# Performance work log

Hardware: AMD Instinct MI355X
Metric: run time of the kernel (lower is better)

The kernel has to match this reference:

```python
import jax, jax.numpy as jnp
import numpy as np

EPS = 1e-5

def _bn(x, g, b):
    # training-mode BatchNorm1d: batch statistics (biased variance), eps=1e-5
    mean = jnp.mean(x, axis=0)
    var = jnp.mean(jnp.square(x - mean), axis=0)
    return (x - mean) * jax.lax.rsqrt(var + EPS) * g + b

def setup_inputs() -> dict:
    key = jax.random.key(0)
    ks = jax.random.split(key, 16)
    n_nodes, n_edges, d_h, d_e = 50000, 800000, 128, 64
    in_feats, h1, h2, out_feats = 2 * d_h + d_e, 256, 128, 1
    def lin(k, fi, fo):
        bound = 1.0 / np.sqrt(fi)
        kw, kb = jax.random.split(k)
        W = jax.random.uniform(kw, (fo, fi), jnp.float32, -bound, bound)
        b = jax.random.uniform(kb, (fo,), jnp.float32, -bound, bound)
        return W, b
    W1, b1 = lin(ks[0], in_feats, h1)
    W2, b2 = lin(ks[1], h1, h2)
    W3, b3 = lin(ks[2], h2, out_feats)
    return {
        "h": jax.random.normal(ks[3], (n_nodes, d_h), jnp.float32),
        "e": jax.random.normal(ks[4], (n_edges, d_e), jnp.float32),
        "src": jax.random.randint(ks[5], (n_edges,), 0, n_nodes, jnp.int32),
        "dst": jax.random.randint(ks[6], (n_edges,), 0, n_nodes, jnp.int32),
        "bn0_g": jnp.ones((in_feats,), jnp.float32), "bn0_b": jnp.zeros((in_feats,), jnp.float32),
        "W1": W1, "b1": b1,
        "bn1_g": jnp.ones((h1,), jnp.float32), "bn1_b": jnp.zeros((h1,), jnp.float32),
        "W2": W2, "b2": b2,
        "bn2_g": jnp.ones((h2,), jnp.float32), "bn2_b": jnp.zeros((h2,), jnp.float32),
        "W3": W3, "b3": b3,
    }

def reference(h, e, src, dst, bn0_g, bn0_b, W1, b1, bn1_g, bn1_b, W2, b2, bn2_g, bn2_b, W3, b3):
    # edge gather + concat: [n_edges, 2*d_h + d_e]
    x = jnp.concatenate([h[src], h[dst], e], axis=1)
    x = _bn(x, bn0_g, bn0_b)
    x = jnp.maximum(x @ W1.T + b1, 0.0)  # Linear + ReLU (dropout = identity, deterministic)
    x = _bn(x, bn1_g, bn1_b)
    x = jnp.maximum(x @ W2.T + b2, 0.0)
    x = _bn(x, bn2_g, bn2_b)
    return x @ W3.T + b3
```

## Files before the change

kernel.cpp:

```cpp
#include <hip/hip_runtime.h>


#define N_EDGES 800000
#define N_NODES 50000

typedef __attribute__((ext_vector_type(8))) short bf8_t;
typedef __attribute__((ext_vector_type(4))) float f4_t;
typedef __attribute__((ext_vector_type(2))) unsigned int u2_t;
typedef __attribute__((ext_vector_type(4))) unsigned int u4_t;

__device__ __forceinline__ unsigned short f2bf(float f) {
    unsigned int u = __builtin_bit_cast(unsigned int, f);
    u += 0x7FFFu + ((u >> 16) & 1u);
    return (unsigned short)(u >> 16);
}
__device__ __forceinline__ float bf2f(unsigned short s) {
    unsigned int u = ((unsigned int)s) << 16;
    return __builtin_bit_cast(float, u);
}
__device__ __forceinline__ unsigned int cvt_pk(float lo, float hi) {
    unsigned int r;
    asm("v_cvt_pk_bf16_f32 %0, %1, %2" : "=v"(r) : "v"(lo), "v"(hi));
    return r;
}
__device__ __forceinline__ bf8_t cvt8(f4_t x, f4_t y) {
    union { unsigned int u[4]; bf8_t v; } r;
    r.u[0] = cvt_pk(x[0], x[1]);
    r.u[1] = cvt_pk(x[2], x[3]);
    r.u[2] = cvt_pk(y[0], y[1]);
    r.u[3] = cvt_pk(y[2], y[3]);
    return r.v;
}

__global__ __launch_bounds__(256) void k_hist(const int* __restrict__ src, const int* __restrict__ dst,
                                              int* __restrict__ cs, int* __restrict__ cd) {
    int i = blockIdx.x * 256 + threadIdx.x;
    if (i < N_EDGES) {
        atomicAdd(&cs[src[i]], 1);
        atomicAdd(&cd[dst[i]], 1);
    }
}

__global__ __launch_bounds__(256) void k_ecvt(const float* __restrict__ e,
        unsigned short* __restrict__ ebf, float* __restrict__ sum, float* __restrict__ sq) {
    const int tid = threadIdx.x;
    const int lane = tid & 63;
    const int cg = tid & 7, rr = tid >> 3;
    f4_t sa = {0.f,0.f,0.f,0.f}, sb = sa, qa = sa, qb = sa;
    for (int r = blockIdx.x * 32 + rr; r < N_EDGES; r += gridDim.x * 32) {
        f4_t va = __builtin_nontemporal_load((const f4_t*)(e + (size_t)r * 64 + cg * 8));
        f4_t vb = __builtin_nontemporal_load((const f4_t*)(e + (size_t)r * 64 + cg * 8 + 4));
        sa += va; qa += va * va; sb += vb; qb += vb * vb;
        bf8_t o = cvt8(va, vb);
        __builtin_nontemporal_store(o,
            (bf8_t*)(ebf + (size_t)(r >> 4) * 1024 + (cg >> 2) * 512 + (((r & 15) << 2) + (cg & 3)) * 8));
    }
#pragma unroll
    for (int d = 8; d <= 32; d <<= 1) {
#pragma unroll
        for (int j = 0; j < 4; ++j) {
            sa[j] += __shfl_xor(sa[j], d); qa[j] += __shfl_xor(qa[j], d);
            sb[j] += __shfl_xor(sb[j], d); qb[j] += __shfl_xor(qb[j], d);
        }
    }
    __shared__ float red[128];
    if (tid < 128) red[tid] = 0.f;
    __syncthreads();
    if (lane < 8) {
#pragma unroll
        for (int j = 0; j < 4; ++j) {
            atomicAdd(&red[lane * 8 + j], sa[j]);
            atomicAdd(&red[lane * 8 + 4 + j], sb[j]);
            atomicAdd(&red[64 + lane * 8 + j], qa[j]);
            atomicAdd(&red[64 + lane * 8 + 4 + j], qb[j]);
        }
    }
    __syncthreads();
    if (tid < 64) atomicAdd(&sum[256 + tid], red[tid]);
    else if (tid < 128) atomicAdd(&sq[256 + tid - 64], red[tid]);
}

__global__ __launch_bounds__(256) void k_hstats(const float* __restrict__ h,
                                                const int* __restrict__ cs, const int* __restrict__ cd,
                                                float* __restrict__ sum, float* __restrict__ sq) {
    const int tid = threadIdx.x;
    const int c = tid & 127, g = tid >> 7;
    float ss = 0.f, qs = 0.f, sd = 0.f, qd = 0.f;
    for (int n = blockIdx.x * 2 + g; n < N_NODES; n += gridDim.x * 2) {
        float v = h[(size_t)n * 128 + c];
        float a = (float)cs[n], b = (float)cd[n];
        ss += a * v; qs += a * v * v;
        sd += b * v; qd += b * v * v;
    }
    __shared__ float red[256];
    red[tid] = ss; __syncthreads();
    if (tid < 128) atomicAdd(&sum[tid], red[tid] + red[tid + 128]);
    __syncthreads();
    red[tid] = qs; __syncthreads();
    if (tid < 128) atomicAdd(&sq[tid], red[tid] + red[tid + 128]);
    __syncthreads();
    red[tid] = sd; __syncthreads();
    if (tid < 128) atomicAdd(&sum[128 + tid], red[tid] + red[tid + 128]);
    __syncthreads();
    red[tid] = qd; __syncthreads();
    if (tid < 128) atomicAdd(&sq[128 + tid], red[tid] + red[tid + 128]);
}

__global__ __launch_bounds__(320) void k_fold0(const float* __restrict__ sum, const float* __restrict__ sq,
        const float* __restrict__ g0, const float* __restrict__ b0,
        float* __restrict__ scale0, float* __restrict__ shift0) {
    int j = threadIdx.x;
    if (j < 320) {
        const float invE = 1.f / (float)N_EDGES;
        float mu = sum[j] * invE;
        float var = sq[j] * invE - mu * mu;
        float sc = g0[j] * rsqrtf(var + 1e-5f);
        scale0[j] = sc;
        shift0[j] = b0[j] - mu * sc;
    }
}

__global__ __launch_bounds__(320) void k_foldW1(const float* __restrict__ W1, const float* __restrict__ b1,
        const float* __restrict__ scale0, const float* __restrict__ shift0,
        unsigned short* __restrict__ W1s, unsigned short* __restrict__ W1d,
        unsigned short* __restrict__ W1e, float* __restrict__ b1p) {
    __shared__ float sc[320], sh[320];
    const int tid = threadIdx.x;
    if (tid < 320) { sc[tid] = scale0[tid]; sh[tid] = shift0[tid]; }
    __syncthreads();
    if (tid < 256) {
        float acc = b1[tid];
        const float* wr = W1 + (size_t)tid * 320;
        for (int j = 0; j < 320; ++j) {
            float wv = wr[j];
            acc += wv * sh[j];
            unsigned short wb = f2bf(wv * sc[j]);
            if (j < 128) W1s[tid * 128 + j] = wb;
            else if (j < 256) W1d[tid * 128 + (j - 128)] = wb;
            else W1e[tid * 64 + (j - 256)] = wb;
        }
        b1p[tid] = acc;
    }
}

__global__ __launch_bounds__(256) void k_P(const float* __restrict__ h,
        const unsigned short* __restrict__ W1s, const unsigned short* __restrict__ W1d,
        unsigned short* __restrict__ Ps, unsigned short* __restrict__ Pd) {
    __shared__ unsigned short tile[16 * 264];
    const int tid = threadIdx.x;
    const int w = tid >> 6, lane = tid & 63, quad = lane >> 4, l15 = lane & 15;
    const unsigned short* W = blockIdx.y ? W1d : W1s;
    unsigned short* P = blockIdx.y ? Pd : Ps;
    const size_t base = (size_t)blockIdx.x * 256;
    bf8_t bfr[4][4];
#pragma unroll
    for (int j = 0; j < 4; ++j) {
        const unsigned short* wp = W + (size_t)((w * 4 + j) * 16 + l15) * 128 + quad * 8;
#pragma unroll
        for (int ks = 0; ks < 4; ++ks) bfr[j][ks] = *(const bf8_t*)(wp + ks * 32);
    }
    const int erow = tid >> 4, ex = tid & 15;
    for (int mc = 0; mc < 16; ++mc) {
        const size_t row0 = base + mc * 16;
        size_t ar = row0 + l15; if (ar >= N_NODES) ar = N_NODES - 1;
        const float* hp = h + ar * 128 + quad * 8;
        bf8_t af[4];
#pragma unroll
        for (int ks = 0; ks < 4; ++ks)
            af[ks] = cvt8(*(const f4_t*)(hp + ks * 32), *(const f4_t*)(hp + ks * 32 + 4));
#pragma unroll
        for (int j = 0; j < 4; ++j) {
            f4_t t = {0.f, 0.f, 0.f, 0.f};
#pragma unroll
            for (int ks = 0; ks < 4; ++ks)
                t = __builtin_amdgcn_mfma_f32_16x16x32_bf16(af[ks], bfr[j][ks], t, 0, 0, 0);
            const unsigned int p01 = cvt_pk(t[0], t[1]);
            const unsigned int p23 = cvt_pk(t[2], t[3]);
            const int col = (w * 4 + j) * 16 + l15;
            tile[(quad * 4 + 0) * 264 + col] = (unsigned short)p01;
            tile[(quad * 4 + 1) * 264 + col] = (unsigned short)(p01 >> 16);
            tile[(quad * 4 + 2) * 264 + col] = (unsigned short)p23;
            tile[(quad * 4 + 3) * 264 + col] = (unsigned short)(p23 >> 16);
        }
        __syncthreads();
        const size_t orow = row0 + erow;
        if (orow < N_NODES) {
            u4_t v0 = *(const u4_t*)(tile + erow * 264 + ex * 16);
            u4_t v1 = *(const u4_t*)(tile + erow * 264 + ex * 16 + 8);
            *(u4_t*)(P + orow * 256 + ex * 16) = v0;
            *(u4_t*)(P + orow * 256 + ex * 16 + 8) = v1;
        }
        __syncthreads();
    }
}

__global__ __launch_bounds__(256) void k_stats1(const unsigned short* __restrict__ ebf,
        const int* __restrict__ src, const int* __restrict__ dst,
        const unsigned short* __restrict__ Ps, const unsigned short* __restrict__ Pd,
        const unsigned short* __restrict__ W1e, const float* __restrict__ b1p,
        float* __restrict__ slots) {
    __shared__ __align__(16) float tile1[2][16 * 268];
    __shared__ int sIdx[256], dIdx[256];
    const int tid = threadIdx.x;
    const int w = tid >> 6, lane = tid & 63, quad = lane >> 4, l15 = lane & 15;
    const int perm = l15 * 4 + quad;
    const size_t base = (size_t)blockIdx.x * 256;
    const size_t blk16 = (size_t)blockIdx.x * 16;
    sIdx[tid] = src[base + tid];
    dIdx[tid] = dst[base + tid];
    bf8_t bfr1[4][2];
    float bias4[4];
#pragma unroll
    for (int j = 0; j < 4; ++j) {
        const unsigned short* wp = W1e + (size_t)((w * 4 + j) * 16 + l15) * 64 + quad * 8;
        bfr1[j][0] = *(const bf8_t*)(wp);
        bfr1[j][1] = *(const bf8_t*)(wp + 32);
        bias4[j] = b1p[(w * 4 + j) * 16 + l15];
    }
    const int erow = tid >> 4, ex = tid & 15;
    float s[16], q[16];
#pragma unroll
    for (int j = 0; j < 16; ++j) { s[j] = 0.f; q[j] = 0.f; }
    __syncthreads();
    bf8_t af0, af1;
    u4_t gs0, gs1, gd0, gd1;
    {
        const unsigned short* ap = ebf + blk16 * 1024 + perm * 8;
        af0 = __builtin_nontemporal_load((const bf8_t*)(ap));
        af1 = __builtin_nontemporal_load((const bf8_t*)(ap + 512));
        const size_t sr = (size_t)sIdx[erow] * 256, dr = (size_t)dIdx[erow] * 256;
        gs0 = *(const u4_t*)(Ps + sr + ex * 8);
        gs1 = *(const u4_t*)(Ps + sr + ex * 8 + 128);
        gd0 = *(const u4_t*)(Pd + dr + ex * 8);
        gd1 = *(const u4_t*)(Pd + dr + ex * 8 + 128);
    }
    for (int mc = 0; mc < 16; ++mc) {
        float* t1 = tile1[mc & 1];
#pragma unroll
        for (int j = 0; j < 4; ++j) {
            f4_t t = {bias4[j], bias4[j], bias4[j], bias4[j]};
            t = __builtin_amdgcn_mfma_f32_16x16x32_bf16(af0, bfr1[j][0], t, 0, 0, 0);
            t = __builtin_amdgcn_mfma_f32_16x16x32_bf16(af1, bfr1[j][1], t, 0, 0, 0);
#pragma unroll
            for (int r = 0; r < 4; ++r)
                t1[(quad * 4 + r) * 268 + (w * 4 + j) * 16 + l15] = t[r];
        }
        if (mc < 15) {
            const unsigned short* ap = ebf + (blk16 + mc + 1) * 1024 + perm * 8;
            af0 = __builtin_nontemporal_load((const bf8_t*)(ap));
            af1 = __builtin_nontemporal_load((const bf8_t*)(ap + 512));
        }
        __syncthreads();
#pragma unroll
        for (int i = 0; i < 2; ++i) {
            const float* tp = t1 + erow * 268 + ex * 8 + 128 * i;
            f4_t tv0 = *(const f4_t*)tp;
            f4_t tv1 = *(const f4_t*)(tp + 4);
            const unsigned short* su = (const unsigned short*)(i ? &gs1 : &gs0);
            const unsigned short* du = (const unsigned short*)(i ? &gd1 : &gd0);
#pragma unroll
            for (int j = 0; j < 4; ++j) {
                float v = fmaxf(tv0[j] + bf2f(su[j]) + bf2f(du[j]), 0.f);
                s[i * 8 + j] += v; q[i * 8 + j] += v * v;
            }
#pragma unroll
            for (int j = 0; j < 4; ++j) {
                float v = fmaxf(tv1[j] + bf2f(su[4 + j]) + bf2f(du[4 + j]), 0.f);
                s[i * 8 + 4 + j] += v; q[i * 8 + 4 + j] += v * v;
            }
        }
        if (mc < 15) {
            const size_t sr = (size_t)sIdx[(mc + 1) * 16 + erow] * 256;
            const size_t dr = (size_t)dIdx[(mc + 1) * 16 + erow] * 256;
            gs0 = *(const u4_t*)(Ps + sr + ex * 8);
            gs1 = *(const u4_t*)(Ps + sr + ex * 8 + 128);
            gd0 = *(const u4_t*)(Pd + dr + ex * 8);
            gd1 = *(const u4_t*)(Pd + dr + ex * 8 + 128);
        }
    }
#pragma unroll
    for (int j = 0; j < 16; ++j) {
        s[j] += __shfl_xor(s[j], 16); s[j] += __shfl_xor(s[j], 32);
        q[j] += __shfl_xor(q[j], 16); q[j] += __shfl_xor(q[j], 32);
    }
    float* scratch = &tile1[0][0];
    if (lane < 16) {
#pragma unroll
        for (int j = 0; j < 16; ++j) {
            scratch[(w * 16 + l15) * 16 + j] = s[j];
            scratch[1024 + (w * 16 + l15) * 16 + j] = q[j];
        }
    }
    __syncthreads();
    {
        const int c = tid;
        const int idx = (c & 7) + (c >> 7) * 8;
        const int exx = (c >> 3) & 15;
        float S = 0.f, Q = 0.f;
#pragma unroll
        for (int ww = 0; ww < 4; ++ww) {
            S += scratch[(ww * 16 + exx) * 16 + idx];
            Q += scratch[1024 + (ww * 16 + exx) * 16 + idx];
        }
        float* sl = slots + (size_t)(blockIdx.x & 63) * 512;
        atomicAdd(&sl[c], S);
        atomicAdd(&sl[256 + c], Q);
    }
}

__global__ __launch_bounds__(256) void k_fold1(const float* __restrict__ slots,
        const float* __restrict__ g1, const float* __restrict__ b1n,
        const float* __restrict__ W2, const float* __restrict__ b2,
        unsigned short* __restrict__ W2p, float* __restrict__ b2p) {
    __shared__ float sc[256], sh[256];
    const int tid = threadIdx.x;
    float S = 0.f, Q = 0.f;
    for (int s = 0; s < 64; ++s) { S += slots[s * 512 + tid]; Q += slots[s * 512 + 256 + tid]; }
    const float invE = 1.f / (float)N_EDGES;
    float mu = S * invE;
    float var = Q * invE - mu * mu;
    float scl = g1[tid] * rsqrtf(var + 1e-5f);
    sc[tid] = scl; sh[tid] = b1n[tid] - mu * scl;
    __syncthreads();
    if (tid < 128) {
        float acc = b2[tid];
        const float* wr = W2 + (size_t)tid * 256;
        for (int j = 0; j < 256; ++j) {
            float wv = wr[j];
            acc += wv * sh[j];
            W2p[tid * 256 + j] = f2bf(wv * sc[j]);
        }
        b2p[tid] = acc;
    }
}

__global__ __launch_bounds__(256) void k_L12(const unsigned short* __restrict__ ebf,
        const int* __restrict__ src, const int* __restrict__ dst,
        const unsigned short* __restrict__ Ps, const unsigned short* __restrict__ Pd,
        const unsigned short* __restrict__ W1e, const float* __restrict__ b1p,
        const unsigned short* __restrict__ W2p, const float* __restrict__ b2p,
        unsigned short* __restrict__ a2c, float* __restrict__ slots) {
    __shared__ __align__(16) float tile1[16 * 268];
    __shared__ unsigned short tile2[2][4096];
    __shared__ int sIdx[256], dIdx[256];
    const int tid = threadIdx.x;
    const int w = tid >> 6, lane = tid & 63, quad = lane >> 4, l15 = lane & 15;
    const int perm = l15 * 4 + quad;
    const size_t base = (size_t)blockIdx.x * 256;
    const size_t blk16 = (size_t)blockIdx.x * 16;
    sIdx[tid] = src[base + tid];
    dIdx[tid] = dst[base + tid];
    bf8_t bfr1[4][2];
    float bias4[4];
#pragma unroll
    for (int j = 0; j < 4; ++j) {
        const unsigned short* wp = W1e + (size_t)((w * 4 + j) * 16 + l15) * 64 + quad * 8;
        bfr1[j][0] = *(const bf8_t*)(wp);
        bfr1[j][1] = *(const bf8_t*)(wp + 32);
        bias4[j] = b1p[(w * 4 + j) * 16 + l15];
    }
    bf8_t bfr2[2][8];
    float bias2[2];
#pragma unroll
    for (int j = 0; j < 2; ++j) {
        const unsigned short* wp = W2p + (size_t)((w * 2 + j) * 16 + l15) * 256 + quad * 8;
#pragma unroll
        for (int ks = 0; ks < 8; ++ks) bfr2[j][ks] = *(const bf8_t*)(wp + ks * 32);
        bias2[j] = b2p[(w * 2 + j) * 16 + l15];
    }
    const int erow = tid >> 4, ex = tid & 15;
    float s0 = 0.f, q0 = 0.f, s1 = 0.f, q1 = 0.f;
    __syncthreads();
    bf8_t af0, af1;
    u4_t gs0, gs1, gd0, gd1;
    {
        const unsigned short* ap = ebf + blk16 * 1024 + perm * 8;
        af0 = __builtin_nontemporal_load((const bf8_t*)(ap));
        af1 = __builtin_nontemporal_load((const bf8_t*)(ap + 512));
        const size_t sr = (size_t)sIdx[erow] * 256, dr = (size_t)dIdx[erow] * 256;
        gs0 = *(const u4_t*)(Ps + sr + ex * 8);
        gs1 = *(const u4_t*)(Ps + sr + ex * 8 + 128);
        gd0 = *(const u4_t*)(Pd + dr + ex * 8);
        gd1 = *(const u4_t*)(Pd + dr + ex * 8 + 128);
    }
    for (int mc = 0; mc < 16; ++mc) {
        unsigned short* t2 = tile2[mc & 1];
#pragma unroll
        for (int j = 0; j < 4; ++j) {
            f4_t t = {bias4[j], bias4[j], bias4[j], bias4[j]};
            t = __builtin_amdgcn_mfma_f32_16x16x32_bf16(af0, bfr1[j][0], t, 0, 0, 0);
            t = __builtin_amdgcn_mfma_f32_16x16x32_bf16(af1, bfr1[j][1], t, 0, 0, 0);
#pragma unroll
            for (int r = 0; r < 4; ++r)
                tile1[(quad * 4 + r) * 268 + (w * 4 + j) * 16 + l15] = t[r];
        }
        if (mc < 15) {
            const unsigned short* ap = ebf + (blk16 + mc + 1) * 1024 + perm * 8;
            af0 = __builtin_nontemporal_load((const bf8_t*)(ap));
            af1 = __builtin_nontemporal_load((const bf8_t*)(ap + 512));
        }
        __syncthreads();
#pragma unroll
        for (int i = 0; i < 2; ++i) {
            const float* tp = tile1 + erow * 268 + ex * 8 + 128 * i;
            f4_t tv0 = *(const f4_t*)tp;
            f4_t tv1 = *(const f4_t*)(tp + 4);
            const unsigned short* su = (const unsigned short*)(i ? &gs1 : &gs0);
            const unsigned short* du = (const unsigned short*)(i ? &gd1 : &gd0);
            float c0 = fmaxf(tv0[0] + bf2f(su[0]) + bf2f(du[0]), 0.f);
            float c1 = fmaxf(tv0[1] + bf2f(su[1]) + bf2f(du[1]), 0.f);
            float c2 = fmaxf(tv0[2] + bf2f(su[2]) + bf2f(du[2]), 0.f);
            float c3 = fmaxf(tv0[3] + bf2f(su[3]) + bf2f(du[3]), 0.f);
            float c4 = fmaxf(tv1[0] + bf2f(su[4]) + bf2f(du[4]), 0.f);
            float c5 = fmaxf(tv1[1] + bf2f(su[5]) + bf2f(du[5]), 0.f);
            float c6 = fmaxf(tv1[2] + bf2f(su[6]) + bf2f(du[6]), 0.f);
            float c7 = fmaxf(tv1[3] + bf2f(su[7]) + bf2f(du[7]), 0.f);
            u4_t ov;
            ov[0] = cvt_pk(c0, c1);
            ov[1] = cvt_pk(c2, c3);
            ov[2] = cvt_pk(c4, c5);
            ov[3] = cvt_pk(c6, c7);
            *(u4_t*)(&t2[((ex >> 2) + 4 * i) * 512 + (erow * 4 + (ex & 3)) * 8]) = ov;
        }
        if (mc < 15) {
            const size_t sr = (size_t)sIdx[(mc + 1) * 16 + erow] * 256;
            const size_t dr = (size_t)dIdx[(mc + 1) * 16 + erow] * 256;
            gs0 = *(const u4_t*)(Ps + sr + ex * 8);
            gs1 = *(const u4_t*)(Ps + sr + ex * 8 + 128);
            gd0 = *(const u4_t*)(Pd + dr + ex * 8);
            gd1 = *(const u4_t*)(Pd + dr + ex * 8 + 128);
        }
        __syncthreads();
        f4_t acc0 = {bias2[0], bias2[0], bias2[0], bias2[0]};
        f4_t acc1 = {bias2[1], bias2[1], bias2[1], bias2[1]};
#pragma unroll
        for (int ks = 0; ks < 8; ++ks) {
            bf8_t a = *(const bf8_t*)(&t2[ks * 512 + perm * 8]);
            acc0 = __builtin_amdgcn_mfma_f32_16x16x32_bf16(a, bfr2[0][ks], acc0, 0, 0, 0);
            acc1 = __builtin_amdgcn_mfma_f32_16x16x32_bf16(a, bfr2[1][ks], acc1, 0, 0, 0);
        }
        unsigned short* outp = a2c + (blk16 + mc) * 2048;
        {
            float v0 = fmaxf(acc0[0], 0.f), v1 = fmaxf(acc0[1], 0.f);
            float v2 = fmaxf(acc0[2], 0.f), v3 = fmaxf(acc0[3], 0.f);
            s0 += v0; q0 += v0 * v0; s0 += v1; q0 += v1 * v1;
            s0 += v2; q0 += v2 * v2; s0 += v3; q0 += v3 * v3;
            u2_t pw; pw[0] = cvt_pk(v0, v1); pw[1] = cvt_pk(v2, v3);
            __builtin_nontemporal_store(pw,
                (u2_t*)(outp + (((w * 2) * 16 + l15) * 4 + quad) * 4));
        }
        {
            float v0 = fmaxf(acc1[0], 0.f), v1 = fmaxf(acc1[1], 0.f);
            float v2 = fmaxf(acc1[2], 0.f), v3 = fmaxf(acc1[3], 0.f);
            s1 += v0; q1 += v0 * v0; s1 += v1; q1 += v1 * v1;
            s1 += v2; q1 += v2 * v2; s1 += v3; q1 += v3 * v3;
            u2_t pw; pw[0] = cvt_pk(v0, v1); pw[1] = cvt_pk(v2, v3);
            __builtin_nontemporal_store(pw,
                (u2_t*)(outp + (((w * 2 + 1) * 16 + l15) * 4 + quad) * 4));
        }
    }
    s0 += __shfl_xor(s0, 16); s0 += __shfl_xor(s0, 32);
    q0 += __shfl_xor(q0, 16); q0 += __shfl_xor(q0, 32);
    s1 += __shfl_xor(s1, 16); s1 += __shfl_xor(s1, 32);
    q1 += __shfl_xor(q1, 16); q1 += __shfl_xor(q1, 32);
    if (lane < 16) {
        float* sl = slots + (size_t)(blockIdx.x & 63) * 256;
        const int c0 = (w * 2) * 16 + l15;
        atomicAdd(&sl[c0], s0); atomicAdd(&sl[128 + c0], q0);
        atomicAdd(&sl[c0 + 16], s1); atomicAdd(&sl[128 + c0 + 16], q1);
    }
}

__global__ __launch_bounds__(128) void k_fold2(const float* __restrict__ slots,
        const float* __restrict__ g2, const float* __restrict__ b2n,
        const float* __restrict__ W3, const float* __restrict__ b3,
        float* __restrict__ w3p, float* __restrict__ b3p) {
    __shared__ float red[128];
    const int tid = threadIdx.x;
    float S = 0.f, Q = 0.f;
    for (int s = 0; s < 64; ++s) { S += slots[s * 256 + tid]; Q += slots[s * 256 + 128 + tid]; }
    const float invE = 1.f / (float)N_EDGES;
    float mu = S * invE;
    float var = Q * invE - mu * mu;
    float scl = g2[tid] * rsqrtf(var + 1e-5f);
    float shf = b2n[tid] - mu * scl;
    w3p[tid] = W3[tid] * scl;
    red[tid] = W3[tid] * shf;
    __syncthreads();
    for (int st = 64; st > 0; st >>= 1) {
        if (tid < st) red[tid] += red[tid + st];
        __syncthreads();
    }
    if (tid == 0) b3p[0] = b3[0] + red[0];
}

__global__ __launch_bounds__(256) void k_L3(const unsigned short* __restrict__ a2c,
        const float* __restrict__ w3p, const float* __restrict__ b3p, float* __restrict__ out) {
    __shared__ float wl[128];
    const int tid = threadIdx.x;
    if (tid < 128) wl[tid] = w3p[tid];
    __syncthreads();
    const int w = tid >> 6, lane = tid & 63, q = lane >> 4, c = lane & 15;
    const float bb = b3p[0];
#pragma unroll
    for (int i = 0; i < 4; ++i) {
        const size_t b = (size_t)blockIdx.x * 16 + w * 4 + i;
        const unsigned short* bp = a2c + b * 2048 + c * 16 + q * 4;
        float a0 = 0.f, a1r = 0.f, a2r = 0.f, a3r = 0.f;
#pragma unroll
        for (int jt = 0; jt < 8; ++jt) {
            u2_t v = __builtin_nontemporal_load((const u2_t*)(bp + jt * 256));
            const unsigned short* u = (const unsigned short*)&v;
            const float wv = wl[jt * 16 + c];
            a0 += bf2f(u[0]) * wv; a1r += bf2f(u[1]) * wv;
            a2r += bf2f(u[2]) * wv; a3r += bf2f(u[3]) * wv;
        }
#pragma unroll
        for (int d = 1; d <= 8; d <<= 1) {
            a0 += __shfl_xor(a0, d); a1r += __shfl_xor(a1r, d);
            a2r += __shfl_xor(a2r, d); a3r += __shfl_xor(a3r, d);
        }
        if (c == 0) {
            f4_t o = {a0 + bb, a1r + bb, a2r + bb, a3r + bb};
            *(f4_t*)(out + b * 16 + q * 4) = o;
        }
    }
}

extern "C" void kernel_launch(void* const* d_in, const int* in_sizes, int n_in,
                              void* d_out, int out_size, void* d_ws, size_t ws_size,
                              hipStream_t stream) {
    (void)in_sizes; (void)n_in; (void)out_size; (void)ws_size;
    const float* h   = (const float*)d_in[0];
    const float* e   = (const float*)d_in[1];
    const int*   src = (const int*)d_in[2];
    const int*   dst = (const int*)d_in[3];
    const float* bn0_g = (const float*)d_in[4];
    const float* bn0_b = (const float*)d_in[5];
    const float* W1 = (const float*)d_in[6];
    const float* b1 = (const float*)d_in[7];
    const float* bn1_g = (const float*)d_in[8];
    const float* bn1_b = (const float*)d_in[9];
    const float* W2 = (const float*)d_in[10];
    const float* b2 = (const float*)d_in[11];
    const float* bn2_g = (const float*)d_in[12];
    const float* bn2_b = (const float*)d_in[13];
    const float* W3 = (const float*)d_in[14];
    const float* b3 = (const float*)d_in[15];

    char* ws = (char*)d_ws;
    size_t off = 0;
    auto alloc = [&](size_t bytes) { char* p = ws + off; off += (bytes + 255) & ~(size_t)255; return p; };
    int*   cnt_s = (int*)alloc((size_t)N_NODES * 4);
    int*   cnt_d = (int*)alloc((size_t)N_NODES * 4);
    float* bn0_sum = (float*)alloc(320 * 4);
    float* bn0_sq  = (float*)alloc(320 * 4);
    float* bn1_slots = (float*)alloc(64 * 512 * 4);
    float* bn2_slots = (float*)alloc(64 * 256 * 4);
    const size_t zero_end = off;
    float* scale0 = (float*)alloc(320 * 4);
    float* shift0 = (float*)alloc(320 * 4);
    unsigned short* W1s = (unsigned short*)alloc(256 * 128 * 2);
    unsigned short* W1d = (unsigned short*)alloc(256 * 128 * 2);
    unsigned short* W1e = (unsigned short*)alloc(256 * 64 * 2);
    float* b1p = (float*)alloc(256 * 4);
    unsigned short* W2p = (unsigned short*)alloc(128 * 256 * 2);
    float* b2p = (float*)alloc(128 * 4);
    float* w3p = (float*)alloc(128 * 4);
    float* b3p = (float*)alloc(4);
    unsigned short* Ps = (unsigned short*)alloc((size_t)N_NODES * 256 * 2);
    unsigned short* Pd = (unsigned short*)alloc((size_t)N_NODES * 256 * 2);
    unsigned short* ebf = (unsigned short*)alloc((size_t)(N_EDGES / 16) * 2048);
    unsigned short* a2c = (unsigned short*)alloc((size_t)(N_EDGES / 16) * 4096);

    hipMemsetAsync(d_ws, 0, zero_end, stream);
    k_hist<<<(N_EDGES + 255) / 256, 256, 0, stream>>>(src, dst, cnt_s, cnt_d);
    k_ecvt<<<1024, 256, 0, stream>>>(e, ebf, bn0_sum, bn0_sq);
    k_hstats<<<400, 256, 0, stream>>>(h, cnt_s, cnt_d, bn0_sum, bn0_sq);
    k_fold0<<<1, 320, 0, stream>>>(bn0_sum, bn0_sq, bn0_g, bn0_b, scale0, shift0);
    k_foldW1<<<1, 320, 0, stream>>>(W1, b1, scale0, shift0, W1s, W1d, W1e, b1p);
    k_P<<<dim3(196, 2), 256, 0, stream>>>(h, W1s, W1d, Ps, Pd);
    k_stats1<<<N_EDGES / 256, 256, 0, stream>>>(ebf, src, dst, Ps, Pd, W1e, b1p, bn1_slots);
    k_fold1<<<1, 256, 0, stream>>>(bn1_slots, bn1_g, bn1_b, W2, b2, W2p, b2p);
    k_L12<<<N_EDGES / 256, 256, 0, stream>>>(ebf, src, dst, Ps, Pd, W1e, b1p, W2p, b2p, a2c, bn2_slots);
    k_fold2<<<1, 128, 0, stream>>>(bn2_slots, bn2_g, bn2_b, W3, b3, w3p, b3p);
    k_L3<<<N_EDGES / 256, 256, 0, stream>>>(a2c, w3p, b3p, (float*)d_out);
}
```

Measured before the change: 987.2 us.

## Fuse histogram into e-conversion, merge BN0 fold, use bf16 layer-1 LDS tiles

The degree histogram moves into the e-to-bf16 conversion kernel, and the BN0 fold is merged into the W1 folding kernel, removing two launches. In k_stats1 and k_L12 the layer-1 intermediate tile in LDS is now stored as bf16 instead of fp32, which halves LDS footprint and read traffic and may raise occupancy, at the cost of an extra rounding step. k_L12 drops its tile2 double buffer and is launched as two halves with a block offset. The bf16 rounding of the pre-activation slightly changes numerics.

```diff
diff --git a/kernel.cpp b/kernel.cpp
--- a/kernel.cpp
+++ b/kernel.cpp
@@ -32,17 +32,10 @@
     return r.v;
 }
 
-__global__ __launch_bounds__(256) void k_hist(const int* __restrict__ src, const int* __restrict__ dst,
-                                              int* __restrict__ cs, int* __restrict__ cd) {
-    int i = blockIdx.x * 256 + threadIdx.x;
-    if (i < N_EDGES) {
-        atomicAdd(&cs[src[i]], 1);
-        atomicAdd(&cd[dst[i]], 1);
-    }
-}
-
 __global__ __launch_bounds__(256) void k_ecvt(const float* __restrict__ e,
-        unsigned short* __restrict__ ebf, float* __restrict__ sum, float* __restrict__ sq) {
+        const int* __restrict__ src, const int* __restrict__ dst,
+        unsigned short* __restrict__ ebf, int* __restrict__ cs, int* __restrict__ cd,
+        float* __restrict__ sum, float* __restrict__ sq) {
     const int tid = threadIdx.x;
     const int lane = tid & 63;
     const int cg = tid & 7, rr = tid >> 3;
@@ -54,6 +47,10 @@
         bf8_t o = cvt8(va, vb);
         __builtin_nontemporal_store(o,
             (bf8_t*)(ebf + (size_t)(r >> 4) * 1024 + (cg >> 2) * 512 + (((r & 15) << 2) + (cg & 3)) * 8));
+        if (cg == 0) {
+            atomicAdd(&cs[src[r]], 1);
+            atomicAdd(&cd[dst[r]], 1);
+        }
     }
 #pragma unroll
     for (int d = 8; d <= 32; d <<= 1) {
@@ -106,27 +103,21 @@
     if (tid < 128) atomicAdd(&sq[128 + tid], red[tid] + red[tid + 128]);
 }
 
-__global__ __launch_bounds__(320) void k_fold0(const float* __restrict__ sum, const float* __restrict__ sq,
+__global__ __launch_bounds__(320) void k_foldW1(const float* __restrict__ sum, const float* __restrict__ sq,
         const float* __restrict__ g0, const float* __restrict__ b0,
-        float* __restrict__ scale0, float* __restrict__ shift0) {
-    int j = threadIdx.x;
-    if (j < 320) {
-        const float invE = 1.f / (float)N_EDGES;
-        float mu = sum[j] * invE;
-        float var = sq[j] * invE - mu * mu;
-        float sc = g0[j] * rsqrtf(var + 1e-5f);
-        scale0[j] = sc;
-        shift0[j] = b0[j] - mu * sc;
-    }
-}
-
-__global__ __launch_bounds__(320) void k_foldW1(const float* __restrict__ W1, const float* __restrict__ b1,
-        const float* __restrict__ scale0, const float* __restrict__ shift0,
+        const float* __restrict__ W1, const float* __restrict__ b1,
         unsigned short* __restrict__ W1s, unsigned short* __restrict__ W1d,
         unsigned short* __restrict__ W1e, float* __restrict__ b1p) {
     __shared__ float sc[320], sh[320];
     const int tid = threadIdx.x;
-    if (tid < 320) { sc[tid] = scale0[tid]; sh[tid] = shift0[tid]; }
+    if (tid < 320) {
+        const float invE = 1.f / (float)N_EDGES;
+        float mu = sum[tid] * invE;
+        float var = sq[tid] * invE - mu * mu;
+        float scl = g0[tid] * rsqrtf(var + 1e-5f);
+        sc[tid] = scl;
+        sh[tid] = b0[tid] - mu * scl;
+    }
     __syncthreads();
     if (tid < 256) {
         float acc = b1[tid];
@@ -199,7 +190,7 @@
         const unsigned short* __restrict__ Ps, const unsigned short* __restrict__ Pd,
         const unsigned short* __restrict__ W1e, const float* __restrict__ b1p,
         float* __restrict__ slots) {
-    __shared__ __align__(16) float tile1[2][16 * 268];
+    __shared__ __align__(16) unsigned short tile1[2][16 * 264];
     __shared__ int sIdx[256], dIdx[256];
     const int tid = threadIdx.x;
     const int w = tid >> 6, lane = tid & 63, quad = lane >> 4, l15 = lane & 15;
@@ -235,15 +226,19 @@
         gd1 = *(const u4_t*)(Pd + dr + ex * 8 + 128);
     }
     for (int mc = 0; mc < 16; ++mc) {
-        float* t1 = tile1[mc & 1];
+        unsigned short* t1 = tile1[mc & 1];
 #pragma unroll
         for (int j = 0; j < 4; ++j) {
             f4_t t = {bias4[j], bias4[j], bias4[j], bias4[j]};
             t = __builtin_amdgcn_mfma_f32_16x16x32_bf16(af0, bfr1[j][0], t, 0, 0, 0);
             t = __builtin_amdgcn_mfma_f32_16x16x32_bf16(af1, bfr1[j][1], t, 0, 0, 0);
-#pragma unroll
-            for (int r = 0; r < 4; ++r)
-                t1[(quad * 4 + r) * 268 + (w * 4 + j) * 16 + l15] = t[r];
+            const unsigned int p01 = cvt_pk(t[0], t[1]);
+            const unsigned int p23 = cvt_pk(t[2], t[3]);
+            const int col = (w * 4 + j) * 16 + l15;
+            t1[(quad * 4 + 0) * 264 + col] = (unsigned short)p01;
+            t1[(quad * 4 + 1) * 264 + col] = (unsigned short)(p01 >> 16);
+            t1[(quad * 4 + 2) * 264 + col] = (unsigned short)p23;
+            t1[(quad * 4 + 3) * 264 + col] = (unsigned short)(p23 >> 16);
         }
         if (mc < 15) {
             const unsigned short* ap = ebf + (blk16 + mc + 1) * 1024 + perm * 8;
@@ -253,20 +248,14 @@
         __syncthreads();
 #pragma unroll
         for (int i = 0; i < 2; ++i) {
-            const float* tp = t1 + erow * 268 + ex * 8 + 128 * i;
-            f4_t tv0 = *(const f4_t*)tp;
-            f4_t tv1 = *(const f4_t*)(tp + 4);
+            u4_t tv = *(const u4_t*)(t1 + erow * 264 + ex * 8 + 128 * i);
+            const unsigned short* tu = (const unsigned short*)&tv;
             const unsigned short* su = (const unsigned short*)(i ? &gs1 : &gs0);
             const unsigned short* du = (const unsigned short*)(i ? &gd1 : &gd0);
 #pragma unroll
-            for (int j = 0; j < 4; ++j) {
-                float v = fmaxf(tv0[j] + bf2f(su[j]) + bf2f(du[j]), 0.f);
+            for (int j = 0; j < 8; ++j) {
+                float v = fmaxf(bf2f(tu[j]) + bf2f(su[j]) + bf2f(du[j]), 0.f);
                 s[i * 8 + j] += v; q[i * 8 + j] += v * v;
-            }
-#pragma unroll
-            for (int j = 0; j < 4; ++j) {
-                float v = fmaxf(tv1[j] + bf2f(su[4 + j]) + bf2f(du[4 + j]), 0.f);
-                s[i * 8 + 4 + j] += v; q[i * 8 + 4 + j] += v * v;
             }
         }
         if (mc < 15) {
@@ -283,7 +272,7 @@
         s[j] += __shfl_xor(s[j], 16); s[j] += __shfl_xor(s[j], 32);
         q[j] += __shfl_xor(q[j], 16); q[j] += __shfl_xor(q[j], 32);
     }
-    float* scratch = &tile1[0][0];
+    float* scratch = (float*)&tile1[0][0];
     if (lane < 16) {
 #pragma unroll
         for (int j = 0; j < 16; ++j) {
@@ -339,15 +328,16 @@
         const unsigned short* __restrict__ Ps, const unsigned short* __restrict__ Pd,
         const unsigned short* __restrict__ W1e, const float* __restrict__ b1p,
         const unsigned short* __restrict__ W2p, const float* __restrict__ b2p,
-        unsigned short* __restrict__ a2c, float* __restrict__ slots) {
-    __shared__ __align__(16) float tile1[16 * 268];
-    __shared__ unsigned short tile2[2][4096];
+        unsigned short* __restrict__ a2c, float* __restrict__ slots, const int bofs) {
+    __shared__ __align__(16) unsigned short tile1[16 * 264];
+    __shared__ __align__(16) unsigned short tile2[4096];
     __shared__ int sIdx[256], dIdx[256];
     const int tid = threadIdx.x;
     const int w = tid >> 6, lane = tid & 63, quad = lane >> 4, l15 = lane & 15;
     const int perm = l15 * 4 + quad;
-    const size_t base = (size_t)blockIdx.x * 256;
-    const size_t blk16 = (size_t)blockIdx.x * 16;
+    const int bid = bofs + blockIdx.x;
+    const size_t base = (size_t)bid * 256;
+    const size_t blk16 = (size_t)bid * 16;
     sIdx[tid] = src[base + tid];
     dIdx[tid] = dst[base + tid];
     bf8_t bfr1[4][2];
@@ -384,15 +374,18 @@
         gd1 = *(const u4_t*)(Pd + dr + ex * 8 + 128);
     }
     for (int mc = 0; mc < 16; ++mc) {
-        unsigned short* t2 = tile2[mc & 1];
 #pragma unroll
         for (int j = 0; j < 4; ++j) {
             f4_t t = {bias4[j], bias4[j], bias4[j], bias4[j]};
             t = __builtin_amdgcn_mfma_f32_16x16x32_bf16(af0, bfr1[j][0], t, 0, 0, 0);
             t = __builtin_amdgcn_mfma_f32_16x16x32_bf16(af1, bfr1[j][1], t, 0, 0, 0);
-#pragma unroll
-            for (int r = 0; r < 4; ++r)
-                tile1[(quad * 4 + r) * 268 + (w * 4 + j) * 16 + l15] = t[r];
+            const unsigned int p01 = cvt_pk(t[0], t[1]);
+            const unsigned int p23 = cvt_pk(t[2], t[3]);
+            const int col = (w * 4 + j) * 16 + l15;
+            tile1[(quad * 4 + 0) * 264 + col] = (unsigned short)p01;
+            tile1[(quad * 4 + 1) * 264 + col] = (unsigned short)(p01 >> 16);
+            tile1[(quad * 4 + 2) * 264 + col] = (unsigned short)p23;
+            tile1[(quad * 4 + 3) * 264 + col] = (unsigned short)(p23 >> 16);
         }
         if (mc < 15) {
             const unsigned short* ap = ebf + (blk16 + mc + 1) * 1024 + perm * 8;
@@ -402,25 +395,24 @@
         __syncthreads();
 #pragma unroll
         for (int i = 0; i < 2; ++i) {
-            const float* tp = tile1 + erow * 268 + ex * 8 + 128 * i;
-            f4_t tv0 = *(const f4_t*)tp;
-            f4_t tv1 = *(const f4_t*)(tp + 4);
+            u4_t tv = *(const u4_t*)(tile1 + erow * 264 + ex * 8 + 128 * i);
+            const unsigned short* tu = (const unsigned short*)&tv;
             const unsigned short* su = (const unsigned short*)(i ? &gs1 : &gs0);
             const unsigned short* du = (const unsigned short*)(i ? &gd1 : &gd0);
-            float c0 = fmaxf(tv0[0] + bf2f(su[0]) + bf2f(du[0]), 0.f);
-            float c1 = fmaxf(tv0[1] + bf2f(su[1]) + bf2f(du[1]), 0.f);
-            float c2 = fmaxf(tv0[2] + bf2f(su[2]) + bf2f(du[2]), 0.f);
-            float c3 = fmaxf(tv0[3] + bf2f(su[3]) + bf2f(du[3]), 0.f);
-            float c4 = fmaxf(tv1[0] + bf2f(su[4]) + bf2f(du[4]), 0.f);
-            float c5 = fmaxf(tv1[1] + bf2f(su[5]) + bf2f(du[5]), 0.f);
-            float c6 = fmaxf(tv1[2] + bf2f(su[6]) + bf2f(du[6]), 0.f);
-            float c7 = fmaxf(tv1[3] + bf2f(su[7]) + bf2f(du[7]), 0.f);
+            float c0 = fmaxf(bf2f(tu[0]) + bf2f(su[0]) + bf2f(du[0]), 0.f);
+            float c1 = fmaxf(bf2f(tu[1]) + bf2f(su[1]) + bf2f(du[1]), 0.f);
+            float c2 = fmaxf(bf2f(tu[2]) + bf2f(su[2]) + bf2f(du[2]), 0.f);
+            float c3 = fmaxf(bf2f(tu[3]) + bf2f(su[3]) + bf2f(du[3]), 0.f);
+            float c4 = fmaxf(bf2f(tu[4]) + bf2f(su[4]) + bf2f(du[4]), 0.f);
+            float c5 = fmaxf(bf2f(tu[5]) + bf2f(su[5]) + bf2f(du[5]), 0.f);
+            float c6 = fmaxf(bf2f(tu[6]) + bf2f(su[6]) + bf2f(du[6]), 0.f);
+            float c7 = fmaxf(bf2f(tu[7]) + bf2f(su[7]) + bf2f(du[7]), 0.f);
             u4_t ov;
             ov[0] = cvt_pk(c0, c1);
             ov[1] = cvt_pk(c2, c3);
             ov[2] = cvt_pk(c4, c5);
             ov[3] = cvt_pk(c6, c7);
-            *(u4_t*)(&t2[((ex >> 2) + 4 * i) * 512 + (erow * 4 + (ex & 3)) * 8]) = ov;
+            *(u4_t*)(&tile2[((ex >> 2) + 4 * i) * 512 + (erow * 4 + (ex & 3)) * 8]) = ov;
         }
         if (mc < 15) {
             const size_t sr = (size_t)sIdx[(mc + 1) * 16 + erow] * 256;
@@ -435,7 +427,7 @@
         f4_t acc1 = {bias2[1], bias2[1], bias2[1], bias2[1]};
 #pragma unroll
         for (int ks = 0; ks < 8; ++ks) {
-            bf8_t a = *(const bf8_t*)(&t2[ks * 512 + perm * 8]);
+            bf8_t a = *(const bf8_t*)(&tile2[ks * 512 + perm * 8]);
             acc0 = __builtin_amdgcn_mfma_f32_16x16x32_bf16(a, bfr2[0][ks], acc0, 0, 0, 0);
             acc1 = __builtin_amdgcn_mfma_f32_16x16x32_bf16(a, bfr2[1][ks], acc1, 0, 0, 0);
         }
@@ -464,7 +456,7 @@
     s1 += __shfl_xor(s1, 16); s1 += __shfl_xor(s1, 32);
     q1 += __shfl_xor(q1, 16); q1 += __shfl_xor(q1, 32);
     if (lane < 16) {
-        float* sl = slots + (size_t)(blockIdx.x & 63) * 256;
+        float* sl = slots + (size_t)(bid & 63) * 256;
         const int c0 = (w * 2) * 16 + l15;
         atomicAdd(&sl[c0], s0); atomicAdd(&sl[128 + c0], q0);
         atomicAdd(&sl[c0 + 16], s1); atomicAdd(&sl[128 + c0 + 16], q1);
@@ -558,8 +550,6 @@
     float* bn1_slots = (float*)alloc(64 * 512 * 4);
     float* bn2_slots = (float*)alloc(64 * 256 * 4);
     const size_t zero_end = off;
-    float* scale0 = (float*)alloc(320 * 4);
-    float* shift0 = (float*)alloc(320 * 4);
     unsigned short* W1s = (unsigned short*)alloc(256 * 128 * 2);
     unsigned short* W1d = (unsigned short*)alloc(256 * 128 * 2);
     unsigned short* W1e = (unsigned short*)alloc(256 * 64 * 2);
@@ -574,15 +564,14 @@
     unsigned short* a2c = (unsigned short*)alloc((size_t)(N_EDGES / 16) * 4096);
 
     hipMemsetAsync(d_ws, 0, zero_end, stream);
-    k_hist<<<(N_EDGES + 255) / 256, 256, 0, stream>>>(src, dst, cnt_s, cnt_d);
-    k_ecvt<<<1024, 256, 0, stream>>>(e, ebf, bn0_sum, bn0_sq);
+    k_ecvt<<<1024, 256, 0, stream>>>(e, src, dst, ebf, cnt_s, cnt_d, bn0_sum, bn0_sq);
     k_hstats<<<400, 256, 0, stream>>>(h, cnt_s, cnt_d, bn0_sum, bn0_sq);
-    k_fold0<<<1, 320, 0, stream>>>(bn0_sum, bn0_sq, bn0_g, bn0_b, scale0, shift0);
-    k_foldW1<<<1, 320, 0, stream>>>(W1, b1, scale0, shift0, W1s, W1d, W1e, b1p);
+    k_foldW1<<<1, 320, 0, stream>>>(bn0_sum, bn0_sq, bn0_g, bn0_b, W1, b1, W1s, W1d, W1e, b1p);
     k_P<<<dim3(196, 2), 256, 0, stream>>>(h, W1s, W1d, Ps, Pd);
     k_stats1<<<N_EDGES / 256, 256, 0, stream>>>(ebf, src, dst, Ps, Pd, W1e, b1p, bn1_slots);
     k_fold1<<<1, 256, 0, stream>>>(bn1_slots, bn1_g, bn1_b, W2, b2, W2p, b2p);
-    k_L12<<<N_EDGES / 256, 256, 0, stream>>>(ebf, src, dst, Ps, Pd, W1e, b1p, W2p, b2p, a2c, bn2_slots);
+    k_L12<<<1562, 256, 0, stream>>>(ebf, src, dst, Ps, Pd, W1e, b1p, W2p, b2p, a2c, bn2_slots, 0);
+    k_L12<<<1563, 256, 0, stream>>>(ebf, src, dst, Ps, Pd, W1e, b1p, W2p, b2p, a2c, bn2_slots, 1562);
     k_fold2<<<1, 128, 0, stream>>>(bn2_slots, bn2_g, bn2_b, W3, b3, w3p, b3p);
     k_L3<<<N_EDGES / 256, 256, 0, stream>>>(a2c, w3p, b3p, (float*)d_out);
 }
```

New measurement: 974.6 us. Within noise of the previous version (-1.3%).
